# Kernel optimization log

Measured on AMD Instinct MI355X. Metric: run time of the kernel, lower is better.

## Reference

```python
import jax, jax.numpy as jnp
import numpy as np

N = 100000   # nodes
E = 1600000  # edges (avg degree 16)
D = 64       # input_dim = hidden_dim = output_dim
BN_EPS = 1e-5
LEAKY_SLOPE = 0.01


def setup_inputs() -> dict:
    key = jax.random.key(0)
    ks = jax.random.split(key, 8)
    s = 1.0 / np.sqrt(D)
    return {
        "x": jax.random.normal(ks[0], (N, D), jnp.float32),
        "edge_index": jax.random.randint(ks[1], (2, E), 0, N, dtype=jnp.int32),
        "W1": jax.random.uniform(ks[2], (D, D), jnp.float32, -s, s),
        "b1": jnp.zeros((D,), jnp.float32),
        "gamma": jnp.ones((D,), jnp.float32),
        "beta": jnp.zeros((D,), jnp.float32),
        "W2": jax.random.uniform(ks[3], (D, D), jnp.float32, -s, s),
        "b2": jnp.zeros((D,), jnp.float32),
    }


def reference(x, edge_index, W1, b1, gamma, beta, W2, b2):
    n = x.shape[0]
    # GCN: add self-loops, symmetric normalization D^-1/2 (A+I) D^-1/2
    loops = jnp.arange(n, dtype=edge_index.dtype)
    src = jnp.concatenate([edge_index[0], loops])
    dst = jnp.concatenate([edge_index[1], loops])
    deg = jax.ops.segment_sum(jnp.ones_like(dst, dtype=x.dtype), dst, num_segments=n)
    dinv = jnp.where(deg > 0, jax.lax.rsqrt(jnp.maximum(deg, 1.0)), 0.0)
    norm = dinv[src] * dinv[dst]  # [E+N]

    def gcn(h, W, b):
        h = h @ W                              # [N, D]
        msg = h[src] * norm[:, None]           # gather + scale, [E+N, D]
        return jax.ops.segment_sum(msg, dst, num_segments=n) + b

    h = gcn(x, W1, b1)
    # BatchNorm1d (training-mode batch stats, biased variance)
    mu = jnp.mean(h, axis=0)
    var = jnp.mean((h - mu) ** 2, axis=0)
    h = gamma * (h - mu) * jax.lax.rsqrt(var + BN_EPS) + beta
    # LeakyReLU; dropout p=0.0 is identity
    h = jnp.where(h >= 0, h, LEAKY_SLOPE * h)
    return gcn(h, W2, b2)
```

## Files before the change

### kernel.cpp

```cpp
#include <hip/hip_runtime.h>
#include <hip/hip_fp16.h>

#define LEAKY 0.01f
#define BN_EPS 1e-5f
#define NB 256
#define NW 256
#define EMAX 7168
#define BCAP 12288

typedef int v4i __attribute__((ext_vector_type(4)));

__global__ __launch_bounds__(256) void k_part(const int* __restrict__ src,
                                              const int* __restrict__ dst,
                                              unsigned* __restrict__ barr,
                                              int* __restrict__ bofs,
                                              int e, int nper) {
  __shared__ int lcnt[NB], lofs[NB], lcur[NB], sd[256];
  int wb = blockIdx.x, t = threadIdx.x;
  int S = (e + NW - 1) / NW;
  int s0 = wb * S, s1 = min(e, s0 + S);
  lcnt[t] = 0;
  lcur[t] = 0;
  __syncthreads();
  for (int i = s0 + t; i < s1; i += 256) atomicAdd(&lcnt[dst[i] / nper], 1);
  __syncthreads();
  int v = lcnt[t];
  sd[t] = v;
  __syncthreads();
  for (int off = 1; off < 256; off <<= 1) {
    int x = (t >= off) ? sd[t - off] : 0;
    __syncthreads();
    sd[t] += x;
    __syncthreads();
  }
  lofs[t] = sd[t] - v;
  bofs[wb * (NB + 1) + t] = sd[t] - v;
  if (t == 255) bofs[wb * (NB + 1) + NB] = sd[255];
  __syncthreads();
  for (int i = s0 + t; i < s1; i += 256) {
    int d = dst[i];
    int b = d / nper;
    int r = atomicAdd(&lcur[b], 1);
    barr[s0 + lofs[b] + r] = ((unsigned)src[i] << 9) | (unsigned)(d - b * nper);
  }
}

__global__ __launch_bounds__(256) void k_csrb(const unsigned* __restrict__ barr,
                                              const int* __restrict__ bofs,
                                              int* __restrict__ csr,
                                              int2* __restrict__ seg2,
                                              float* __restrict__ dinv,
                                              int n, int nper, int e) {
  __shared__ int eds[EMAX];
  __shared__ int cnt_[512];
  __shared__ int base_[512];
  __shared__ int sd[256];
  __shared__ int ssz[256], soff[256], sstart[256];
  int b = blockIdx.x, t = threadIdx.x;
  int S = (e + NW - 1) / NW;
  int lo = b * nper;
  int nn = min(nper, n - lo);
  if (nn < 0) nn = 0;
  int st_ = bofs[t * (NB + 1) + b];
  int en_ = bofs[t * (NB + 1) + b + 1];
  int v = en_ - st_;
  sstart[t] = st_;
  ssz[t] = v;
  sd[t] = v;
  __syncthreads();
  for (int off = 1; off < 256; off <<= 1) {
    int x = (t >= off) ? sd[t - off] : 0;
    __syncthreads();
    sd[t] += x;
    __syncthreads();
  }
  soff[t] = sd[t] - v;
  __syncthreads();
  int total = min(sd[255], EMAX);
  int wv = t >> 6, lane = t & 63;
  for (int wb = wv; wb < NW; wb += 4) {
    int sz = ssz[wb], of = soff[wb];
    const unsigned* rp = barr + (size_t)wb * S + sstart[wb];
    for (int k = lane; k < sz && of + k < EMAX; k += 64) eds[of + k] = (int)rp[k];
  }
  cnt_[t] = 0;
  cnt_[t + 256] = 0;
  __syncthreads();
  for (int i = t; i < total; i += 256) atomicAdd(&cnt_[eds[i] & 511], 1);
  __syncthreads();
  int c0 = cnt_[2 * t], c1 = cnt_[2 * t + 1];
  int p0 = (2 * t < nn) ? ((c0 + 15) & ~15) : 0;
  int p1 = (2 * t + 1 < nn) ? ((c1 + 15) & ~15) : 0;
  int ts = p0 + p1;
  sd[t] = ts;
  __syncthreads();
  for (int off = 1; off < 256; off <<= 1) {
    int x = (t >= off) ? sd[t - off] : 0;
    __syncthreads();
    sd[t] += x;
    __syncthreads();
  }
  int run = sd[t] - ts;
  base_[2 * t] = run;
  base_[2 * t + 1] = run + p0;
  __syncthreads();
  int bb = b * BCAP;
  for (int i = t; i < nn; i += 256) {
    int c = cnt_[i];
    int pc = (c + 15) & ~15;
    int ba = bb + base_[i];
    seg2[lo + i] = make_int2(ba, ba + pc);
    dinv[lo + i] = rsqrtf((float)(c + 1));
    for (int j = c; j < pc; j++) csr[ba + j] = n;
  }
  __syncthreads();
  cnt_[t] = 0;
  cnt_[t + 256] = 0;
  __syncthreads();
  for (int i = t; i < total; i += 256) {
    int vv = eds[i];
    int lcl = vv & 511;
    int r = atomicAdd(&cnt_[lcl], 1);
    csr[bb + base_[lcl] + r] = vv >> 9;
  }
  if (b == 0 && t == 0) dinv[n] = 0.f;
}

template <bool BN>
__global__ __launch_bounds__(256) void k_gemm(const float* __restrict__ X,
                                              const float* __restrict__ W,
                                              __half* __restrict__ Y, int n,
                                              const float* __restrict__ dinv,
                                              const double* __restrict__ st,
                                              const float* __restrict__ gamma,
                                              const float* __restrict__ beta) {
  __shared__ float Ws[64][68];
  __shared__ float Xs[64][68];
  __shared__ float smu[64], sisd[64];
  int t = threadIdx.x;
  if (BN) {
    if (t < 64) {
      double mu = st[t] / n;
      double var = st[64 + t] / n - mu * mu;
      smu[t] = (float)mu;
      sisd[t] = (float)(1.0 / sqrt(var + (double)BN_EPS));
    }
    __syncthreads();
  }
  int rowbase = blockIdx.x * 64;
#pragma unroll
  for (int p = 0; p < 4; p++) {
    int idx = (p * 256 + t) * 4;
    int r = idx >> 6, c = idx & 63;
    float4 wv = *(const float4*)&W[idx];
    *(float4*)&Ws[r][c] = wv;
    int gr = rowbase + r;
    float4 v = (gr < n) ? *(const float4*)&X[(size_t)gr * 64 + c]
                        : make_float4(0.f, 0.f, 0.f, 0.f);
    if (BN) {
      float* vp = (float*)&v;
#pragma unroll
      for (int q = 0; q < 4; q++) {
        float z = gamma[c + q] * (vp[q] - smu[c + q]) * sisd[c + q] + beta[c + q];
        vp[q] = (z >= 0.f) ? z : LEAKY * z;
      }
    }
    *(float4*)&Xs[r][c] = v;
  }
  __syncthreads();
  int r = t >> 2;
  int cq = t & 3;
  float acc[16];
#pragma unroll
  for (int j = 0; j < 16; j++) acc[j] = 0.f;
#pragma unroll 4
  for (int k = 0; k < 64; k++) {
    float xv = Xs[r][k];
#pragma unroll
    for (int j = 0; j < 16; j++) acc[j] += xv * Ws[k][cq * 16 + j];
  }
  int gr = rowbase + r;
  if (gr < n) {
    float dv = dinv[gr];
    __half2 h2[8];
#pragma unroll
    for (int j = 0; j < 8; j++)
      h2[j] = __floats2half2_rn(acc[2 * j] * dv, acc[2 * j + 1] * dv);
    __half* yp = &Y[(size_t)gr * 64 + cq * 16];
    *(int4*)yp = *(int4*)&h2[0];
    *(int4*)(yp + 8) = *(int4*)&h2[4];
  }
}

__global__ __launch_bounds__(256) void k_agg(const __half* __restrict__ H,
                                             float* __restrict__ O,
                                             const int2* __restrict__ seg2,
                                             const int* __restrict__ csr,
                                             const float* __restrict__ dinv,
                                             const float* __restrict__ bias, int n) {
  int wave = (blockIdx.x * 256 + threadIdx.x) >> 6;
  int lane = threadIdx.x & 63;
  int i = wave;
  if (i >= n) return;
  float di = dinv[i];
  int2 sg = seg2[i];
  int s0 = sg.x, s1 = sg.y;
  int m = lane & 31;
  bool loA = lane < 32;
  float2 sf = __half22float2(*(const __half2*)&H[(size_t)i * 64 + 2 * m]);
  float a0 = loA ? sf.x : 0.f;
  float a1 = loA ? sf.y : 0.f;
  const v4i* cp = (const v4i*)csr;
  int j = s0 >> 2, jend = s1 >> 2;
  v4i q0 = cp[j];
  v4i q1 = cp[j + 1];
  v4i q2 = cp[j + 2];
  v4i q3 = cp[j + 3];
  for (; j < jend; j += 4) {
    v4i p0 = cp[j + 4];
    v4i p1 = cp[j + 5];
    v4i p2 = cp[j + 6];
    v4i p3 = cp[j + 7];
    int i0 = loA ? q0[0] : q0[1];
    int i1 = loA ? q0[2] : q0[3];
    int i2 = loA ? q1[0] : q1[1];
    int i3 = loA ? q1[2] : q1[3];
    int i4 = loA ? q2[0] : q2[1];
    int i5 = loA ? q2[2] : q2[3];
    int i6 = loA ? q3[0] : q3[1];
    int i7 = loA ? q3[2] : q3[3];
    float2 f0 = __half22float2(*(const __half2*)&H[(size_t)i0 * 64 + 2 * m]);
    float2 f1 = __half22float2(*(const __half2*)&H[(size_t)i1 * 64 + 2 * m]);
    float2 f2 = __half22float2(*(const __half2*)&H[(size_t)i2 * 64 + 2 * m]);
    float2 f3 = __half22float2(*(const __half2*)&H[(size_t)i3 * 64 + 2 * m]);
    float2 f4 = __half22float2(*(const __half2*)&H[(size_t)i4 * 64 + 2 * m]);
    float2 f5 = __half22float2(*(const __half2*)&H[(size_t)i5 * 64 + 2 * m]);
    float2 f6 = __half22float2(*(const __half2*)&H[(size_t)i6 * 64 + 2 * m]);
    float2 f7 = __half22float2(*(const __half2*)&H[(size_t)i7 * 64 + 2 * m]);
    a0 += f0.x + f1.x + f2.x + f3.x;
    a1 += f0.y + f1.y + f2.y + f3.y;
    a0 += f4.x + f5.x + f6.x + f7.x;
    a1 += f4.y + f5.y + f6.y + f7.y;
    q0 = p0;
    q1 = p1;
    q2 = p2;
    q3 = p3;
  }
  a0 += __shfl_xor(a0, 32, 64);
  a1 += __shfl_xor(a1, 32, 64);
  if (loA) {
    float2 bv = *(const float2*)&bias[2 * m];
    float2 o;
    o.x = di * a0 + bv.x;
    o.y = di * a1 + bv.y;
    *(float2*)&O[(size_t)i * 64 + 2 * m] = o;
  }
}

__global__ __launch_bounds__(256) void k_bnstats(const float* __restrict__ H,
                                                 double* __restrict__ st, int n) {
  __shared__ double ls[4][64], lss[4][64];
  int lane = threadIdx.x & 63;
  int w = threadIdx.x >> 6;
  int rw = blockIdx.x * 4 + w;
  int nrw = gridDim.x * 4;
  double s = 0.0, ss = 0.0;
  for (int r = rw; r < n; r += nrw) {
    float v = H[(size_t)r * 64 + lane];
    s += v;
    ss += (double)v * v;
  }
  ls[w][lane] = s;
  lss[w][lane] = ss;
  __syncthreads();
  if (w == 0) {
    double a = ls[0][lane] + ls[1][lane] + ls[2][lane] + ls[3][lane];
    double b = lss[0][lane] + lss[1][lane] + lss[2][lane] + lss[3][lane];
    atomicAdd(&st[lane], a);
    atomicAdd(&st[64 + lane], b);
  }
}

extern "C" void kernel_launch(void* const* d_in, const int* in_sizes, int n_in,
                              void* d_out, int out_size, void* d_ws, size_t ws_size,
                              hipStream_t stream) {
  const float* x     = (const float*)d_in[0];
  const int*   ei    = (const int*)d_in[1];
  const float* W1    = (const float*)d_in[2];
  const float* b1    = (const float*)d_in[3];
  const float* gamma = (const float*)d_in[4];
  const float* beta  = (const float*)d_in[5];
  const float* W2    = (const float*)d_in[6];
  const float* b2    = (const float*)d_in[7];
  float* out = (float*)d_out;

  int n = in_sizes[0] / 64;
  int e = in_sizes[1] / 2;
  const int* srcv = ei;
  const int* dstv = ei + e;
  int nper = (n + NB - 1) / NB;

  char* ws = (char*)d_ws;
  size_t p = 0;
  auto alloc = [&](size_t bytes) {
    void* r = ws + p;
    p += (bytes + 255) & ~(size_t)255;
    return r;
  };
  unsigned* barr = (unsigned*)alloc((size_t)(e + 256) * 4);
  int*      bofs = (int*)alloc((size_t)NW * (NB + 1) * 4);
  int*      csr  = (int*)alloc(((size_t)NB * BCAP + 256) * 4);
  int2*     seg2 = (int2*)alloc((size_t)n * 8);
  float*    dinv = (float*)alloc((size_t)(n + 1) * 4);
  double*   st   = (double*)alloc(128 * 8);
  __half*   A    = (__half*)alloc((size_t)(n + 1) * 64 * 2);
  float*    B    = (float*)alloc((size_t)n * 64 * 4);

  hipMemsetAsync(st, 0, 128 * 8, stream);
  hipMemsetAsync(A + (size_t)n * 64, 0, 128, stream);

  int gG = (n + 63) / 64;
  int gAgg = (n + 3) / 4;

  k_part<<<NW, 256, 0, stream>>>(srcv, dstv, barr, bofs, e, nper);
  k_csrb<<<NB, 256, 0, stream>>>(barr, bofs, csr, seg2, dinv, n, nper, e);

  k_gemm<false><<<gG, 256, 0, stream>>>(x, W1, A, n, dinv, nullptr, nullptr, nullptr);
  k_agg<<<gAgg, 256, 0, stream>>>(A, B, seg2, csr, dinv, b1, n);
  k_bnstats<<<256, 256, 0, stream>>>(B, st, n);
  k_gemm<true><<<gG, 256, 0, stream>>>(B, W2, A, n, dinv, st, gamma, beta);
  k_agg<<<gAgg, 256, 0, stream>>>(A, out, seg2, csr, dinv, b2, n);
}
```

Baseline: 224.4 us.

## Store intermediate layer activations in fp16 and fold memsets into kernels

The first aggregation now writes its output in half precision, and the BN-stats and second GEMM kernels read fp16. This halves the traffic of the intermediate buffer across three kernels. The two hipMemsetAsync calls are replaced by zeroing inside k_part and k_csrb, which removes launch overhead. The edge-copy loop in k_csrb now uses half-waves per source bucket to spread the small per-bucket copies. The cost is reduced precision of the pre-BN activations, which could shift the batch statistics slightly.

```diff
diff --git a/kernel.cpp b/kernel.cpp
--- a/kernel.cpp
+++ b/kernel.cpp
@@ -14,9 +14,11 @@
                                               const int* __restrict__ dst,
                                               unsigned* __restrict__ barr,
                                               int* __restrict__ bofs,
+                                              double* __restrict__ st,
                                               int e, int nper) {
   __shared__ int lcnt[NB], lofs[NB], lcur[NB], sd[256];
   int wb = blockIdx.x, t = threadIdx.x;
+  if (wb == 0 && t < 128) st[t] = 0.0;
   int S = (e + NW - 1) / NW;
   int s0 = wb * S, s1 = min(e, s0 + S);
   lcnt[t] = 0;
@@ -50,6 +52,7 @@
                                               int* __restrict__ csr,
                                               int2* __restrict__ seg2,
                                               float* __restrict__ dinv,
+                                              unsigned* __restrict__ Asent,
                                               int n, int nper, int e) {
   __shared__ int eds[EMAX];
   __shared__ int cnt_[512];
@@ -57,6 +60,7 @@
   __shared__ int sd[256];
   __shared__ int ssz[256], soff[256], sstart[256];
   int b = blockIdx.x, t = threadIdx.x;
+  if (b == 0 && t < 32) Asent[t] = 0u;
   int S = (e + NW - 1) / NW;
   int lo = b * nper;
   int nn = min(nper, n - lo);
@@ -78,10 +82,11 @@
   __syncthreads();
   int total = min(sd[255], EMAX);
   int wv = t >> 6, lane = t & 63;
-  for (int wb = wv; wb < NW; wb += 4) {
+  int half = lane >> 5, l32 = lane & 31;
+  for (int wb = wv * 2 + half; wb < NW; wb += 8) {
     int sz = ssz[wb], of = soff[wb];
     const unsigned* rp = barr + (size_t)wb * S + sstart[wb];
-    for (int k = lane; k < sz && of + k < EMAX; k += 64) eds[of + k] = (int)rp[k];
+    for (int k = l32; k < sz && of + k < EMAX; k += 32) eds[of + k] = (int)rp[k];
   }
   cnt_[t] = 0;
   cnt_[t + 256] = 0;
@@ -127,7 +132,7 @@
 }
 
 template <bool BN>
-__global__ __launch_bounds__(256) void k_gemm(const float* __restrict__ X,
+__global__ __launch_bounds__(256) void k_gemm(const void* __restrict__ Xv,
                                               const float* __restrict__ W,
                                               __half* __restrict__ Y, int n,
                                               const float* __restrict__ dinv,
@@ -151,21 +156,46 @@
 #pragma unroll
   for (int p = 0; p < 4; p++) {
     int idx = (p * 256 + t) * 4;
-    int r = idx >> 6, c = idx & 63;
-    float4 wv = *(const float4*)&W[idx];
-    *(float4*)&Ws[r][c] = wv;
-    int gr = rowbase + r;
-    float4 v = (gr < n) ? *(const float4*)&X[(size_t)gr * 64 + c]
-                        : make_float4(0.f, 0.f, 0.f, 0.f);
-    if (BN) {
-      float* vp = (float*)&v;
-#pragma unroll
-      for (int q = 0; q < 4; q++) {
+    *(float4*)&Ws[idx >> 6][idx & 63] = *(const float4*)&W[idx];
+  }
+  if (BN) {
+    const __half* Xh = (const __half*)Xv;
+#pragma unroll
+    for (int p = 0; p < 2; p++) {
+      int idx = (p * 256 + t) * 8;
+      int r = idx >> 6, c = idx & 63;
+      int gr = rowbase + r;
+      float vp[8];
+      if (gr < n) {
+        int4 hv = *(const int4*)&Xh[(size_t)gr * 64 + c];
+        __half2* hp = (__half2*)&hv;
+#pragma unroll
+        for (int q = 0; q < 4; q++) {
+          float2 f = __half22float2(hp[q]);
+          vp[2 * q] = f.x;
+          vp[2 * q + 1] = f.y;
+        }
+      } else {
+#pragma unroll
+        for (int q = 0; q < 8; q++) vp[q] = 0.f;
+      }
+#pragma unroll
+      for (int q = 0; q < 8; q++) {
         float z = gamma[c + q] * (vp[q] - smu[c + q]) * sisd[c + q] + beta[c + q];
-        vp[q] = (z >= 0.f) ? z : LEAKY * z;
+        Xs[r][c + q] = (z >= 0.f) ? z : LEAKY * z;
       }
     }
-    *(float4*)&Xs[r][c] = v;
+  } else {
+    const float* X = (const float*)Xv;
+#pragma unroll
+    for (int p = 0; p < 4; p++) {
+      int idx = (p * 256 + t) * 4;
+      int r = idx >> 6, c = idx & 63;
+      int gr = rowbase + r;
+      float4 v = (gr < n) ? *(const float4*)&X[(size_t)gr * 64 + c]
+                          : make_float4(0.f, 0.f, 0.f, 0.f);
+      *(float4*)&Xs[r][c] = v;
+    }
   }
   __syncthreads();
   int r = t >> 2;
@@ -192,8 +222,9 @@
   }
 }
 
+template <bool FP16OUT>
 __global__ __launch_bounds__(256) void k_agg(const __half* __restrict__ H,
-                                             float* __restrict__ O,
+                                             void* __restrict__ Optr,
                                              const int2* __restrict__ seg2,
                                              const int* __restrict__ csr,
                                              const float* __restrict__ dinv,
@@ -250,34 +281,52 @@
   a1 += __shfl_xor(a1, 32, 64);
   if (loA) {
     float2 bv = *(const float2*)&bias[2 * m];
-    float2 o;
-    o.x = di * a0 + bv.x;
-    o.y = di * a1 + bv.y;
-    *(float2*)&O[(size_t)i * 64 + 2 * m] = o;
-  }
-}
-
-__global__ __launch_bounds__(256) void k_bnstats(const float* __restrict__ H,
+    float o0 = di * a0 + bv.x;
+    float o1 = di * a1 + bv.y;
+    if constexpr (FP16OUT) {
+      ((__half2*)Optr)[(size_t)i * 32 + m] = __floats2half2_rn(o0, o1);
+    } else {
+      float2 o;
+      o.x = o0;
+      o.y = o1;
+      *(float2*)&((float*)Optr)[(size_t)i * 64 + 2 * m] = o;
+    }
+  }
+}
+
+__global__ __launch_bounds__(256) void k_bnstats(const __half* __restrict__ H,
                                                  double* __restrict__ st, int n) {
-  __shared__ double ls[4][64], lss[4][64];
-  int lane = threadIdx.x & 63;
-  int w = threadIdx.x >> 6;
-  int rw = blockIdx.x * 4 + w;
-  int nrw = gridDim.x * 4;
-  double s = 0.0, ss = 0.0;
-  for (int r = rw; r < n; r += nrw) {
-    float v = H[(size_t)r * 64 + lane];
-    s += v;
-    ss += (double)v * v;
-  }
-  ls[w][lane] = s;
-  lss[w][lane] = ss;
-  __syncthreads();
-  if (w == 0) {
-    double a = ls[0][lane] + ls[1][lane] + ls[2][lane] + ls[3][lane];
-    double b = lss[0][lane] + lss[1][lane] + lss[2][lane] + lss[3][lane];
-    atomicAdd(&st[lane], a);
-    atomicAdd(&st[64 + lane], b);
+  __shared__ double ds0[8][32], ds1[8][32], dq0[8][32], dq1[8][32];
+  int t = threadIdx.x;
+  int m = t & 31;
+  int g = t >> 5;
+  double s0 = 0.0, s1 = 0.0, q0 = 0.0, q1 = 0.0;
+  const __half2* H2 = (const __half2*)H;
+  for (int r = blockIdx.x * 8 + g; r < n; r += gridDim.x * 8) {
+    float2 f = __half22float2(H2[(size_t)r * 32 + m]);
+    s0 += f.x;
+    s1 += f.y;
+    q0 += (double)f.x * f.x;
+    q1 += (double)f.y * f.y;
+  }
+  ds0[g][m] = s0;
+  ds1[g][m] = s1;
+  dq0[g][m] = q0;
+  dq1[g][m] = q1;
+  __syncthreads();
+  if (g == 0) {
+    double a0 = 0, a1 = 0, b0 = 0, b1 = 0;
+#pragma unroll
+    for (int j = 0; j < 8; j++) {
+      a0 += ds0[j][m];
+      a1 += ds1[j][m];
+      b0 += dq0[j][m];
+      b1 += dq1[j][m];
+    }
+    atomicAdd(&st[2 * m], a0);
+    atomicAdd(&st[2 * m + 1], a1);
+    atomicAdd(&st[64 + 2 * m], b0);
+    atomicAdd(&st[64 + 2 * m + 1], b1);
   }
 }
 
@@ -314,20 +363,18 @@
   float*    dinv = (float*)alloc((size_t)(n + 1) * 4);
   double*   st   = (double*)alloc(128 * 8);
   __half*   A    = (__half*)alloc((size_t)(n + 1) * 64 * 2);
-  float*    B    = (float*)alloc((size_t)n * 64 * 4);
-
-  hipMemsetAsync(st, 0, 128 * 8, stream);
-  hipMemsetAsync(A + (size_t)n * 64, 0, 128, stream);
+  __half*   B    = (__half*)alloc((size_t)n * 64 * 2);
 
   int gG = (n + 63) / 64;
   int gAgg = (n + 3) / 4;
 
-  k_part<<<NW, 256, 0, stream>>>(srcv, dstv, barr, bofs, e, nper);
-  k_csrb<<<NB, 256, 0, stream>>>(barr, bofs, csr, seg2, dinv, n, nper, e);
+  k_part<<<NW, 256, 0, stream>>>(srcv, dstv, barr, bofs, st, e, nper);
+  k_csrb<<<NB, 256, 0, stream>>>(barr, bofs, csr, seg2, dinv,
+                                 (unsigned*)(A + (size_t)n * 64), n, nper, e);
 
   k_gemm<false><<<gG, 256, 0, stream>>>(x, W1, A, n, dinv, nullptr, nullptr, nullptr);
-  k_agg<<<gAgg, 256, 0, stream>>>(A, B, seg2, csr, dinv, b1, n);
+  k_agg<true><<<gAgg, 256, 0, stream>>>(A, B, seg2, csr, dinv, b1, n);
   k_bnstats<<<256, 256, 0, stream>>>(B, st, n);
   k_gemm<true><<<gG, 256, 0, stream>>>(B, W2, A, n, dinv, st, gamma, beta);
-  k_agg<<<gAgg, 256, 0, stream>>>(A, out, seg2, csr, dinv, b2, n);
-}
+  k_agg<false><<<gAgg, 256, 0, stream>>>(A, out, seg2, csr, dinv, b2, n);
+}
```

Result: faster. 203.0 us (-9.5%).
